# Optimization experiments

Measured on AMD Instinct MI355X. Metric: run time of the kernel, lower is better.

## Reference

```python
import jax, jax.numpy as jnp
import numpy as np

W_DIM = 512
CHANNELS = 1024
SIZE = 64            # H = W = 64
SAMPLING_RATE = 64.0
BANDWIDTH = 2.0


def setup_inputs() -> dict:
    key = jax.random.key(0)
    k_w, k_f, k_p, k_wt, k_aw = jax.random.split(key, 5)
    B = 16
    w = jax.random.normal(k_w, (B, W_DIM), dtype=jnp.float32)
    # freqs init as in SynthesisInput.__init__
    freqs = jax.random.normal(k_f, (CHANNELS, 2), dtype=jnp.float32)
    radii = jnp.sqrt(jnp.sum(freqs ** 2, axis=1, keepdims=True))
    freqs = freqs / (radii * jnp.exp(radii ** 2) ** 0.25) * BANDWIDTH
    phases = jax.random.uniform(k_p, (CHANNELS,), dtype=jnp.float32) - 0.5
    weight = jax.random.normal(k_wt, (CHANNELS, CHANNELS), dtype=jnp.float32)
    # affine FC layer (weight_init=0 in original; use small random for a useful test)
    affine_w = jax.random.normal(k_aw, (4, W_DIM), dtype=jnp.float32) * 0.1
    affine_b = jnp.array([1.0, 0.0, 0.0, 0.0], dtype=jnp.float32)
    return {"w": w, "freqs": freqs, "phases": phases, "weight": weight,
            "affine_w": affine_w, "affine_b": affine_b}


def _forward(w, freqs, phases, weight, affine_w, affine_b):
    B = w.shape[0]
    C = freqs.shape[0]
    H = Wd = SIZE
    # affine: FullyConnectedLayer gain = 1/sqrt(in_features)
    t = w @ affine_w.T / jnp.sqrt(jnp.float32(W_DIM)) + affine_b  # [B,4]
    t = t / jnp.linalg.norm(t[:, :2], axis=1, keepdims=True)
    c, s = t[:, 0], t[:, 1]
    # rotation block of m_r (identity base transform, so transform_ = m_r @ m_t)
    R = jnp.stack([jnp.stack([c, -s], -1), jnp.stack([s, c], -1)], -2)  # [B,2,2]
    # translation column: transform_[:, :2, 2] = R @ (-t[:,2:4])
    trans_col = -jnp.einsum('bij,bj->bi', R, t[:, 2:4])                 # [B,2]
    phases_b = phases[None, :] + jnp.einsum('cd,bd->bc', freqs, trans_col)  # [B,C]
    freqs_b = jnp.einsum('cd,bde->bce', freqs, R)                           # [B,C,2]
    amps = jnp.clip(
        1.0 - (jnp.linalg.norm(freqs_b, axis=2) - BANDWIDTH)
        / (SAMPLING_RATE / 2 - BANDWIDTH), 0.0, 1.0)                        # [B,C]
    # affine_grid (align_corners=False): normalized coords (2i+1)/N - 1, scaled
    sx = 0.5 * Wd / SAMPLING_RATE
    sy = 0.5 * H / SAMPLING_RATE
    u = ((jnp.arange(Wd, dtype=jnp.float32) + 0.5) / Wd * 2.0 - 1.0) * sx  # x (width)
    v = ((jnp.arange(H, dtype=jnp.float32) + 0.5) / H * 2.0 - 1.0) * sy    # y (height)
    grid = jnp.stack(jnp.meshgrid(u, v, indexing='xy'), axis=-1)           # [H,W,2]
    x = jnp.einsum('hwd,bcd->bhwc', grid, freqs_b) + phases_b[:, None, None, :]
    x = jnp.sin(x * (2.0 * jnp.pi)) * amps[:, None, None, :]
    x = jnp.einsum('bhwc,kc->bhwk', x, weight / jnp.sqrt(jnp.float32(C)))
    return jnp.transpose(x, (0, 3, 1, 2))  # [B,C,H,W]


def reference(w, freqs, phases, weight, affine_w, affine_b):
    return _forward(w, freqs, phases, weight, affine_w, affine_b)
```

## Files before the change

### kernel.cpp

```cpp
#include <hip/hip_runtime.h>

typedef __attribute__((ext_vector_type(4))) float f32x4;
typedef __attribute__((ext_vector_type(8))) short s16x8;
typedef __attribute__((ext_vector_type(8))) unsigned short u16x8;

#define W_DIM   512
#define CHANNELS 1024
#define SPATIAL 4096
#define NB      16

__device__ inline unsigned short f2bf(float x){
  unsigned int u = __float_as_uint(x);
  u += 0x7fffu + ((u >> 16) & 1u);
  return (unsigned short)(u >> 16);
}

__device__ inline float sin2pi(float x){
  return __builtin_amdgcn_sinf(__builtin_amdgcn_fractf(x));
}
__device__ inline float cos2pi(float x){
  return __builtin_amdgcn_cosf(__builtin_amdgcn_fractf(x));
}

__device__ inline void async_load16(const unsigned short* g, unsigned short* l){
  __builtin_amdgcn_global_load_lds(
      (const __attribute__((address_space(1))) void*)g,
      (__attribute__((address_space(3))) void*)l, 16, 0, 0);
}

__global__ void sy_setup(const float* __restrict__ w, const float* __restrict__ freqs,
                         const float* __restrict__ phases, const float* __restrict__ affine_w,
                         const float* __restrict__ affine_b, float4* __restrict__ params){
  int b = blockIdx.x;
  int t = threadIdx.x;
  float p0=0.f, p1=0.f, p2=0.f, p3=0.f;
  #pragma unroll
  for (int it = 0; it < 2; ++it){
    int i = t + it*256;
    float wv = w[b*W_DIM + i];
    p0 += wv * affine_w[0*W_DIM + i];
    p1 += wv * affine_w[1*W_DIM + i];
    p2 += wv * affine_w[2*W_DIM + i];
    p3 += wv * affine_w[3*W_DIM + i];
  }
  #pragma unroll
  for (int off = 32; off >= 1; off >>= 1){
    p0 += __shfl_down(p0, off);
    p1 += __shfl_down(p1, off);
    p2 += __shfl_down(p2, off);
    p3 += __shfl_down(p3, off);
  }
  __shared__ float red[4][4];
  __shared__ float sc[4];
  int wave = t >> 6, lane = t & 63;
  if (lane == 0){ red[wave][0]=p0; red[wave][1]=p1; red[wave][2]=p2; red[wave][3]=p3; }
  __syncthreads();
  if (t == 0){
    const float inv_sq = 0.04419417382415922f;
    float tv[4];
    #pragma unroll
    for (int j=0;j<4;++j){
      float s = red[0][j]+red[1][j]+red[2][j]+red[3][j];
      tv[j] = s * inv_sq + affine_b[j];
    }
    float n  = sqrtf(tv[0]*tv[0] + tv[1]*tv[1]);
    float iv = 1.0f / n;
    float c = tv[0]*iv, s = tv[1]*iv;
    float t2 = tv[2]*iv, t3 = tv[3]*iv;
    float tcx = -(c*t2 - s*t3);
    float tcy = -(s*t2 + c*t3);
    sc[0]=c; sc[1]=s; sc[2]=tcx; sc[3]=tcy;
  }
  __syncthreads();
  float c = sc[0], s = sc[1], tcx = sc[2], tcy = sc[3];
  #pragma unroll
  for (int j = 0; j < 4; ++j){
    int ci = t + j*256;
    float f0x = freqs[ci*2], f0y = freqs[ci*2+1];
    float fx =  f0x*c + f0y*s;
    float fy = -f0x*s + f0y*c;
    float ph = phases[ci] + f0x*tcx + f0y*tcy;
    float r  = sqrtf(fx*fx + fy*fy);
    float amp = 1.0f - (r - 2.0f) * (1.0f/30.0f);
    amp = fminf(fmaxf(amp, 0.0f), 1.0f);
    float4 P; P.x=fx; P.y=fy; P.z=ph; P.w=amp;
    params[b*CHANNELS + ci] = P;
  }
}

__global__ void sy_cvtw(const float* __restrict__ wt, unsigned short* __restrict__ Wbf){
  int i = (blockIdx.x*256 + threadIdx.x)*4;
  float4 v = *(const float4*)(wt + i);
  ushort4 o;
  o.x = f2bf(v.x*0.03125f); o.y = f2bf(v.y*0.03125f);
  o.z = f2bf(v.z*0.03125f); o.w = f2bf(v.w*0.03125f);
  *(ushort4*)(Wbf + i) = o;
}

__global__ void sy_genS(const float4* __restrict__ params, unsigned short* __restrict__ Sbf,
                        int b0){
  int blk = blockIdx.x;
  int bb  = blk >> 7;
  int b   = b0 + bb;
  int m0  = (blk & 127) * 32;
  int t   = threadIdx.x;
  int c0  = (t & 127) * 8;
  int mh  = t >> 7;
  int h   = m0 >> 6;
  int w0  = (m0 + mh*16) & 63;
  float v  = (h  + 0.5f) * (1.0f/64.0f) - 0.5f;
  float u0 = (w0 + 0.5f) * (1.0f/64.0f) - 0.5f;

  float sU[8], cU[8], sV[8], cV[8], sD[8], cD[8];
  #pragma unroll
  for (int j = 0; j < 8; ++j){
    float4 P = params[b*CHANNELS + c0 + j];
    float V = v*P.y + P.z;
    sV[j] = sin2pi(V) * P.w;
    cV[j] = cos2pi(V) * P.w;
    float U = u0*P.x;
    sU[j] = sin2pi(U);
    cU[j] = cos2pi(U);
    float D = P.x * (1.0f/64.0f);
    sD[j] = sin2pi(D);
    cD[j] = cos2pi(D);
  }

  unsigned short* dst = Sbf + ((size_t)bb * SPATIAL + m0 + mh*16) * CHANNELS + c0;
  for (int im = 0; im < 16; ++im){
    u16x8 o;
    #pragma unroll
    for (int j = 0; j < 8; ++j){
      float val = sU[j]*cV[j] + cU[j]*sV[j];
      o[j] = f2bf(val);
      float ns = sU[j]*cD[j] + cU[j]*sD[j];
      float nc = cU[j]*cD[j] - sU[j]*sD[j];
      sU[j] = ns; cU[j] = nc;
    }
    *(u16x8*)(dst + (size_t)im * CHANNELS) = o;
  }
}

__global__ __launch_bounds__(512, 4) void sy_gemm(const unsigned short* __restrict__ Wbf,
                                                  const unsigned short* __restrict__ Sbf,
                                                  float* __restrict__ out, int b0){
  __shared__ __align__(16) unsigned short lds[3][12288];
  const int tid  = threadIdx.x;
  const int lane = tid & 63, wave = tid >> 6;
  const int wm = wave >> 1, wn = wave & 1;

  const int nwg = gridDim.x;
  const int cpx = nwg >> 3;
  const int bid = blockIdx.x;
  const int sbid = (bid & 7)*cpx + (bid >> 3);
  const int mt  = sbid & 3;
  const int ntl = sbid >> 2;
  const size_t NcolL = (size_t)ntl * 128;
  const int bbl = (int)(NcolL >> 12);
  const int nin = (int)(NcolL & 4095);
  const unsigned short* Abase = Wbf + (size_t)mt * 256 * CHANNELS;
  const unsigned short* Bbase = Sbf + NcolL * CHANNELS;

  int voffA[2], loffA[2];
  #pragma unroll
  for (int j = 0; j < 2; ++j){
    int p   = j*512 + tid;
    int row = p >> 2;
    int kc  = (p & 3) ^ ((row >> 1) & 3);
    voffA[j] = row*CHANNELS + kc*8;
    loffA[j] = p*8;
  }
  int voffB, loffB;
  {
    int p   = tid;
    int row = p >> 2;
    int kc  = (p & 3) ^ ((row >> 1) & 3);
    voffB   = row*CHANNELS + kc*8;
    loffB   = 8192 + p*8;
  }

  const int l15 = lane & 15, kg = lane >> 4;
  const int xs  = (kg ^ ((l15 >> 1) & 3)) * 8;
  const int aoff =        (wm*64 + l15)*32 + xs;
  const int boff = 8192 + (wn*64 + l15)*32 + xs;

  f32x4 acc[4][4];
  #pragma unroll
  for (int i=0;i<4;++i)
    #pragma unroll
    for (int j=0;j<4;++j){
      f32x4 z = {0.f,0.f,0.f,0.f};
      acc[i][j] = z;
    }

  auto STAGE = [&](int kt, int s){
    const int ko = kt * 32;
    unsigned short* l = &lds[s][0];
    async_load16(Abase + voffA[0] + ko, l + loffA[0]);
    async_load16(Abase + voffA[1] + ko, l + loffA[1]);
    async_load16(Bbase + voffB   + ko, l + loffB);
  };
  auto COMPUTE = [&](int s){
    const unsigned short* l = &lds[s][0];
    s16x8 af[4], bv[4];
    #pragma unroll
    for (int i=0;i<4;++i) af[i] = *(const s16x8*)&l[aoff + i*512];
    #pragma unroll
    for (int j=0;j<4;++j) bv[j] = *(const s16x8*)&l[boff + j*512];
    __builtin_amdgcn_s_setprio(1);
    #pragma unroll
    for (int i=0;i<4;++i)
      #pragma unroll
      for (int j=0;j<4;++j)
        acc[i][j] = __builtin_amdgcn_mfma_f32_16x16x32_bf16(af[i], bv[j], acc[i][j], 0, 0, 0);
    __builtin_amdgcn_s_setprio(0);
  };

  STAGE(0, 0); STAGE(1, 1);
  asm volatile("s_waitcnt vmcnt(3)" ::: "memory");
  __builtin_amdgcn_s_barrier();

  int sc = 0, ss = 2;
  for (int t = 0; t < 30; ++t){
    STAGE(t + 2, ss);
    COMPUTE(sc);
    asm volatile("s_waitcnt vmcnt(3)" ::: "memory");
    __builtin_amdgcn_s_barrier();
    sc = (sc == 2) ? 0 : sc + 1;
    ss = (ss == 2) ? 0 : ss + 1;
  }
  COMPUTE(sc);
  asm volatile("s_waitcnt vmcnt(0)" ::: "memory");
  __builtin_amdgcn_s_barrier();
  COMPUTE(1);

  float* outb = out + (size_t)(b0 + bbl) * CHANNELS * SPATIAL;
  const int colb = nin + wn*64 + l15;
  const int row0 = mt*256 + wm*64 + (kg << 2);
  #pragma unroll
  for (int mf = 0; mf < 4; ++mf)
    #pragma unroll
    for (int nf = 0; nf < 4; ++nf)
      #pragma unroll
      for (int r = 0; r < 4; ++r)
        outb[(size_t)(row0 + mf*16 + r) * SPATIAL + colb + nf*16] = acc[mf][nf][r];
}

__global__ void sy_fallback(const float* __restrict__ weight, const float4* __restrict__ params,
                            float* __restrict__ out){
  extern __shared__ float S[];
  int b  = blockIdx.x >> 7;
  int m0 = (blockIdx.x & 127) * 32;
  int t  = threadIdx.x;
  {
    int c0 = t*4;
    float4 P0 = params[b*CHANNELS+c0+0], P1 = params[b*CHANNELS+c0+1];
    float4 P2 = params[b*CHANNELS+c0+2], P3 = params[b*CHANNELS+c0+3];
    int h = m0 >> 6;
    float v = (h + 0.5f)*(1.0f/64.0f) - 0.5f;
    float a0 = v*P0.y+P0.z, a1 = v*P1.y+P1.z, a2 = v*P2.y+P2.z, a3 = v*P3.y+P3.z;
    for (int im = 0; im < 32; ++im){
      int wv = (m0+im) & 63;
      float u = (wv+0.5f)*(1.0f/64.0f) - 0.5f;
      float* row = S + im*CHANNELS + c0;
      row[0] = sin2pi(u*P0.x+a0)*P0.w;
      row[1] = sin2pi(u*P1.x+a1)*P1.w;
      row[2] = sin2pi(u*P2.x+a2)*P2.w;
      row[3] = sin2pi(u*P3.x+a3)*P3.w;
    }
  }
  __syncthreads();
  for (int oi = t; oi < 32*1024; oi += 256){
    int k = oi >> 5, im = oi & 31;
    const float4* wr = (const float4*)(weight + (size_t)k*CHANNELS);
    const float4* sr = (const float4*)(S + im*CHANNELS);
    float sum = 0.f;
    for (int c4 = 0; c4 < CHANNELS/4; ++c4){
      float4 a = wr[c4], s4 = sr[c4];
      sum += a.x*s4.x + a.y*s4.y + a.z*s4.z + a.w*s4.w;
    }
    out[((size_t)b*CHANNELS + k)*SPATIAL + m0 + im] = sum * 0.03125f;
  }
}

extern "C" void kernel_launch(void* const* d_in, const int* in_sizes, int n_in,
                              void* d_out, int out_size, void* d_ws, size_t ws_size,
                              hipStream_t stream){
  const float* w        = (const float*)d_in[0];
  const float* freqs    = (const float*)d_in[1];
  const float* phases   = (const float*)d_in[2];
  const float* weight   = (const float*)d_in[3];
  const float* affine_w = (const float*)d_in[4];
  const float* affine_b = (const float*)d_in[5];
  float* out = (float*)d_out;

  char* ws = (char*)d_ws;
  float4* params = (float4*)ws;
  const size_t off_w = 262144;
  const size_t off_s = off_w + 2097152;
  unsigned short* Wbf = (unsigned short*)(ws + off_w);
  unsigned short* Sbf = (unsigned short*)(ws + off_s);
  const size_t per_batch = (size_t)SPATIAL * CHANNELS * 2;

  sy_setup<<<NB, 256, 0, stream>>>(w, freqs, phases, affine_w, affine_b, params);

  int G = 0;
  if (ws_size >= off_s + per_batch){
    size_t avail = (ws_size - off_s) / per_batch;
    G = avail >= (size_t)NB ? NB : (int)avail;
  }
  if (G == 0){
    sy_fallback<<<NB*128, 256, 32*1024*4, stream>>>(weight, params, out);
    return;
  }
  sy_cvtw<<<1024, 256, 0, stream>>>(weight, Wbf);
  for (int b0 = 0; b0 < NB; b0 += G){
    int g = (NB - b0) < G ? (NB - b0) : G;
    sy_genS<<<g*128, 256, 0, stream>>>(params, Sbf, b0);
    sy_gemm<<<g*128, 512, 0, stream>>>(Wbf, Sbf, out, b0);
  }
}
```

Before: 439.3 us.

## Fuse sinusoid feature generation into GEMM producer, drop global S buffer

Removes the separate sy_genS kernel and its 128 MB bf16 intermediate. Each GEMM workgroup now computes its B-operand tile of sin features directly into shared memory, one K-slice per iteration, using the rotation recurrence. The GEMM tile also grows from 256x128 to 256x256 with a 4-deep A buffer and a 2-deep B buffer, and occupancy drops to 2 workgroups. This saves the global write and reread of the feature matrix, at the cost of per-iteration transcendental work, scattered 2-byte LDS stores and higher register pressure from 32 accumulators per wave.

Result: no change. 440.3 us (+0.2%).

```diff
diff --git a/kernel.cpp b/kernel.cpp
--- a/kernel.cpp
+++ b/kernel.cpp
@@ -2,7 +2,6 @@
 
 typedef __attribute__((ext_vector_type(4))) float f32x4;
 typedef __attribute__((ext_vector_type(8))) short s16x8;
-typedef __attribute__((ext_vector_type(8))) unsigned short u16x8;
 
 #define W_DIM   512
 #define CHANNELS 1024
@@ -97,57 +96,14 @@
   *(ushort4*)(Wbf + i) = o;
 }
 
-__global__ void sy_genS(const float4* __restrict__ params, unsigned short* __restrict__ Sbf,
-                        int b0){
-  int blk = blockIdx.x;
-  int bb  = blk >> 7;
-  int b   = b0 + bb;
-  int m0  = (blk & 127) * 32;
-  int t   = threadIdx.x;
-  int c0  = (t & 127) * 8;
-  int mh  = t >> 7;
-  int h   = m0 >> 6;
-  int w0  = (m0 + mh*16) & 63;
-  float v  = (h  + 0.5f) * (1.0f/64.0f) - 0.5f;
-  float u0 = (w0 + 0.5f) * (1.0f/64.0f) - 0.5f;
-
-  float sU[8], cU[8], sV[8], cV[8], sD[8], cD[8];
-  #pragma unroll
-  for (int j = 0; j < 8; ++j){
-    float4 P = params[b*CHANNELS + c0 + j];
-    float V = v*P.y + P.z;
-    sV[j] = sin2pi(V) * P.w;
-    cV[j] = cos2pi(V) * P.w;
-    float U = u0*P.x;
-    sU[j] = sin2pi(U);
-    cU[j] = cos2pi(U);
-    float D = P.x * (1.0f/64.0f);
-    sD[j] = sin2pi(D);
-    cD[j] = cos2pi(D);
-  }
-
-  unsigned short* dst = Sbf + ((size_t)bb * SPATIAL + m0 + mh*16) * CHANNELS + c0;
-  for (int im = 0; im < 16; ++im){
-    u16x8 o;
-    #pragma unroll
-    for (int j = 0; j < 8; ++j){
-      float val = sU[j]*cV[j] + cU[j]*sV[j];
-      o[j] = f2bf(val);
-      float ns = sU[j]*cD[j] + cU[j]*sD[j];
-      float nc = cU[j]*cD[j] - sU[j]*sD[j];
-      sU[j] = ns; cU[j] = nc;
-    }
-    *(u16x8*)(dst + (size_t)im * CHANNELS) = o;
-  }
-}
-
-__global__ __launch_bounds__(512, 4) void sy_gemm(const unsigned short* __restrict__ Wbf,
-                                                  const unsigned short* __restrict__ Sbf,
-                                                  float* __restrict__ out, int b0){
-  __shared__ __align__(16) unsigned short lds[3][12288];
+__global__ __launch_bounds__(512, 2) void sy_gemm(const unsigned short* __restrict__ Wbf,
+                                                  const float4* __restrict__ params,
+                                                  float* __restrict__ out){
+  __shared__ __align__(16) unsigned short ldsA[4][8192];
+  __shared__ __align__(16) unsigned short ldsB[2][8192];
   const int tid  = threadIdx.x;
   const int lane = tid & 63, wave = tid >> 6;
-  const int wm = wave >> 1, wn = wave & 1;
+  const int wm = wave >> 2, wn = wave & 3;
 
   const int nwg = gridDim.x;
   const int cpx = nwg >> 3;
@@ -155,90 +111,116 @@
   const int sbid = (bid & 7)*cpx + (bid >> 3);
   const int mt  = sbid & 3;
   const int ntl = sbid >> 2;
-  const size_t NcolL = (size_t)ntl * 128;
-  const int bbl = (int)(NcolL >> 12);
+  const size_t NcolL = (size_t)ntl * 256;
+  const int b   = (int)(NcolL >> 12);
   const int nin = (int)(NcolL & 4095);
   const unsigned short* Abase = Wbf + (size_t)mt * 256 * CHANNELS;
-  const unsigned short* Bbase = Sbf + NcolL * CHANNELS;
-
-  int voffA[2], loffA[2];
+
+  int voff[2], loff[2];
   #pragma unroll
   for (int j = 0; j < 2; ++j){
-    int p   = j*512 + tid;
+    int p   = (j*8 + wave)*64 + lane;
     int row = p >> 2;
     int kc  = (p & 3) ^ ((row >> 1) & 3);
-    voffA[j] = row*CHANNELS + kc*8;
-    loffA[j] = p*8;
-  }
-  int voffB, loffB;
-  {
-    int p   = tid;
-    int row = p >> 2;
-    int kc  = (p & 3) ^ ((row >> 1) & 3);
-    voffB   = row*CHANNELS + kc*8;
-    loffB   = 8192 + p*8;
-  }
+    voff[j] = row*CHANNELS + kc*8;
+    loff[j] = p*8;
+  }
+
+  const int chl  = tid & 31;
+  const int hw   = tid >> 5;
+  const int hloc = hw >> 2, wseg = hw & 3;
+  const int colbase = hloc*64 + wseg*16;
+  const int hglob = (nin >> 6) + hloc;
+  const float v  = (hglob + 0.5f)*(1.0f/64.0f) - 0.5f;
+  const float u0 = (wseg*16 + 0.5f)*(1.0f/64.0f) - 0.5f;
+  const int ch7 = chl & 7, cgc = chl >> 3;
+  const float4* Pb = params + (size_t)b*CHANNELS + chl;
 
   const int l15 = lane & 15, kg = lane >> 4;
   const int xs  = (kg ^ ((l15 >> 1) & 3)) * 8;
-  const int aoff =        (wm*64 + l15)*32 + xs;
-  const int boff = 8192 + (wn*64 + l15)*32 + xs;
-
-  f32x4 acc[4][4];
-  #pragma unroll
-  for (int i=0;i<4;++i)
+  const int aoff = (wm*128 + l15)*32 + xs;
+  const int boff = (wn*64  + l15)*32 + xs;
+
+  f32x4 acc[8][4];
+  #pragma unroll
+  for (int i=0;i<8;++i)
     #pragma unroll
     for (int j=0;j<4;++j){
       f32x4 z = {0.f,0.f,0.f,0.f};
       acc[i][j] = z;
     }
 
-  auto STAGE = [&](int kt, int s){
-    const int ko = kt * 32;
-    unsigned short* l = &lds[s][0];
-    async_load16(Abase + voffA[0] + ko, l + loffA[0]);
-    async_load16(Abase + voffA[1] + ko, l + loffA[1]);
-    async_load16(Bbase + voffB   + ko, l + loffB);
+  auto STAGE = [&](int kt){
+    const int ko = kt*32;
+    unsigned short* la = &ldsA[kt & 3][0];
+    async_load16(Abase + voff[0] + ko, la + loff[0]);
+    async_load16(Abase + voff[1] + ko, la + loff[1]);
   };
-  auto COMPUTE = [&](int s){
-    const unsigned short* l = &lds[s][0];
-    s16x8 af[4], bv[4];
-    #pragma unroll
-    for (int i=0;i<4;++i) af[i] = *(const s16x8*)&l[aoff + i*512];
-    #pragma unroll
-    for (int j=0;j<4;++j) bv[j] = *(const s16x8*)&l[boff + j*512];
+  auto SGEN = [&](int kt){
+    float4 P = Pb[kt*32];
+    float V  = v*P.y + P.z;
+    float sV = sin2pi(V)*P.w, cV = cos2pi(V)*P.w;
+    float U  = u0*P.x;
+    float sU = sin2pi(U), cU = cos2pi(U);
+    float D  = P.x * (1.0f/64.0f);
+    float sD = sin2pi(D), cD = cos2pi(D);
+    unsigned short* bl = &ldsB[kt & 1][0];
+    #pragma unroll
+    for (int i = 0; i < 16; ++i){
+      int col = colbase + i;
+      int cl  = cgc ^ ((col >> 1) & 3);
+      bl[col*32 + cl*8 + ch7] = f2bf(sU*cV + cU*sV);
+      float ns = sU*cD + cU*sD;
+      float nc = cU*cD - sU*sD;
+      sU = ns; cU = nc;
+    }
+  };
+  auto COMPUTE = [&](int sA, int sB){
+    s16x8 af[8], bv[4];
+    #pragma unroll
+    for (int mf=0; mf<8; ++mf) af[mf] = *(const s16x8*)&ldsA[sA][aoff + mf*512];
+    #pragma unroll
+    for (int nf=0; nf<4; ++nf) bv[nf] = *(const s16x8*)&ldsB[sB][boff + nf*512];
     __builtin_amdgcn_s_setprio(1);
     #pragma unroll
-    for (int i=0;i<4;++i)
+    for (int mf=0; mf<8; ++mf)
       #pragma unroll
-      for (int j=0;j<4;++j)
-        acc[i][j] = __builtin_amdgcn_mfma_f32_16x16x32_bf16(af[i], bv[j], acc[i][j], 0, 0, 0);
+      for (int nf=0; nf<4; ++nf)
+        acc[mf][nf] = __builtin_amdgcn_mfma_f32_16x16x32_bf16(af[mf], bv[nf], acc[mf][nf], 0, 0, 0);
     __builtin_amdgcn_s_setprio(0);
   };
 
-  STAGE(0, 0); STAGE(1, 1);
-  asm volatile("s_waitcnt vmcnt(3)" ::: "memory");
+  SGEN(0);
+  STAGE(0); STAGE(1); STAGE(2);
+  asm volatile("s_waitcnt lgkmcnt(0)" ::: "memory");
+  asm volatile("s_waitcnt vmcnt(4)"   ::: "memory");
   __builtin_amdgcn_s_barrier();
 
-  int sc = 0, ss = 2;
-  for (int t = 0; t < 30; ++t){
-    STAGE(t + 2, ss);
-    COMPUTE(sc);
-    asm volatile("s_waitcnt vmcnt(3)" ::: "memory");
+  for (int t = 0; t < 29; ++t){
+    SGEN(t + 1);
+    STAGE(t + 3);
+    COMPUTE(t & 3, t & 1);
+    asm volatile("s_waitcnt lgkmcnt(0)" ::: "memory");
+    asm volatile("s_waitcnt vmcnt(4)"   ::: "memory");
     __builtin_amdgcn_s_barrier();
-    sc = (sc == 2) ? 0 : sc + 1;
-    ss = (ss == 2) ? 0 : ss + 1;
-  }
-  COMPUTE(sc);
-  asm volatile("s_waitcnt vmcnt(0)" ::: "memory");
+  }
+  SGEN(30);
+  COMPUTE(29 & 3, 29 & 1);
+  asm volatile("s_waitcnt lgkmcnt(0)" ::: "memory");
+  asm volatile("s_waitcnt vmcnt(2)"   ::: "memory");
   __builtin_amdgcn_s_barrier();
-  COMPUTE(1);
-
-  float* outb = out + (size_t)(b0 + bbl) * CHANNELS * SPATIAL;
+  SGEN(31);
+  COMPUTE(30 & 3, 30 & 1);
+  asm volatile("s_waitcnt lgkmcnt(0)" ::: "memory");
+  asm volatile("s_waitcnt vmcnt(0)"   ::: "memory");
+  __builtin_amdgcn_s_barrier();
+  COMPUTE(31 & 3, 31 & 1);
+
+  float* outb = out + (size_t)b * CHANNELS * SPATIAL;
   const int colb = nin + wn*64 + l15;
-  const int row0 = mt*256 + wm*64 + (kg << 2);
-  #pragma unroll
-  for (int mf = 0; mf < 4; ++mf)
+  const int row0 = mt*256 + wm*128 + (kg << 2);
+  #pragma unroll
+  for (int mf = 0; mf < 8; ++mf)
     #pragma unroll
     for (int nf = 0; nf < 4; ++nf)
       #pragma unroll
@@ -297,26 +279,14 @@
   char* ws = (char*)d_ws;
   float4* params = (float4*)ws;
   const size_t off_w = 262144;
-  const size_t off_s = off_w + 2097152;
   unsigned short* Wbf = (unsigned short*)(ws + off_w);
-  unsigned short* Sbf = (unsigned short*)(ws + off_s);
-  const size_t per_batch = (size_t)SPATIAL * CHANNELS * 2;
 
   sy_setup<<<NB, 256, 0, stream>>>(w, freqs, phases, affine_w, affine_b, params);
 
-  int G = 0;
-  if (ws_size >= off_s + per_batch){
-    size_t avail = (ws_size - off_s) / per_batch;
-    G = avail >= (size_t)NB ? NB : (int)avail;
-  }
-  if (G == 0){
+  if (ws_size >= off_w + 2097152){
+    sy_cvtw<<<1024, 256, 0, stream>>>(weight, Wbf);
+    sy_gemm<<<NB*64, 512, 0, stream>>>(Wbf, params, out);
+  } else {
     sy_fallback<<<NB*128, 256, 32*1024*4, stream>>>(weight, params, out);
-    return;
-  }
-  sy_cvtw<<<1024, 256, 0, stream>>>(weight, Wbf);
-  for (int b0 = 0; b0 < NB; b0 += G){
-    int g = (NB - b0) < G ? (NB - b0) : G;
-    sy_genS<<<g*128, 256, 0, stream>>>(params, Sbf, b0);
-    sy_gemm<<<g*128, 512, 0, stream>>>(Wbf, Sbf, out, b0);
-  }
-}
+  }
+}
```

## Enlarge GEMM tile to 256x256 with 4-stage LDS pipeline

Applied to the files above, without the earlier changes.

Doubles the GEMM block's N tile from 128 to 256 columns, giving each wave a 128x64 sub-tile with 32 accumulators, and halves the grid. The LDS ring goes from 3 to 4 stages with a 3-deep prefetch, so loads run further ahead of compute. Each tile load is reused across more MFMAs, but register pressure rises (launch bounds cut to 2 blocks per CU), occupancy drops, and there are fewer workgroups to spread across CUs.

Measured after the change: 428.5 us. 2.5% less time.

```diff
diff --git a/kernel.cpp b/kernel.cpp
--- a/kernel.cpp
+++ b/kernel.cpp
@@ -141,13 +141,13 @@
   }
 }
 
-__global__ __launch_bounds__(512, 4) void sy_gemm(const unsigned short* __restrict__ Wbf,
+__global__ __launch_bounds__(512, 2) void sy_gemm(const unsigned short* __restrict__ Wbf,
                                                   const unsigned short* __restrict__ Sbf,
                                                   float* __restrict__ out, int b0){
-  __shared__ __align__(16) unsigned short lds[3][12288];
+  __shared__ __align__(16) unsigned short lds[4][2][8192];
   const int tid  = threadIdx.x;
   const int lane = tid & 63, wave = tid >> 6;
-  const int wm = wave >> 1, wn = wave & 1;
+  const int wm = wave >> 2, wn = wave & 3;
 
   const int nwg = gridDim.x;
   const int cpx = nwg >> 3;
@@ -155,90 +155,84 @@
   const int sbid = (bid & 7)*cpx + (bid >> 3);
   const int mt  = sbid & 3;
   const int ntl = sbid >> 2;
-  const size_t NcolL = (size_t)ntl * 128;
+  const size_t NcolL = (size_t)ntl * 256;
   const int bbl = (int)(NcolL >> 12);
   const int nin = (int)(NcolL & 4095);
   const unsigned short* Abase = Wbf + (size_t)mt * 256 * CHANNELS;
   const unsigned short* Bbase = Sbf + NcolL * CHANNELS;
 
-  int voffA[2], loffA[2];
+  int voff[2], loff[2];
   #pragma unroll
   for (int j = 0; j < 2; ++j){
-    int p   = j*512 + tid;
+    int p   = (j*8 + wave)*64 + lane;
     int row = p >> 2;
-    int kc  = (p & 3) ^ ((row >> 1) & 3);
-    voffA[j] = row*CHANNELS + kc*8;
-    loffA[j] = p*8;
-  }
-  int voffB, loffB;
-  {
-    int p   = tid;
-    int row = p >> 2;
-    int kc  = (p & 3) ^ ((row >> 1) & 3);
-    voffB   = row*CHANNELS + kc*8;
-    loffB   = 8192 + p*8;
+    int kcg = (p & 3) ^ ((row >> 1) & 3);
+    voff[j] = row*CHANNELS + kcg*8;
+    loff[j] = p*8;
   }
 
   const int l15 = lane & 15, kg = lane >> 4;
   const int xs  = (kg ^ ((l15 >> 1) & 3)) * 8;
-  const int aoff =        (wm*64 + l15)*32 + xs;
-  const int boff = 8192 + (wn*64 + l15)*32 + xs;
-
-  f32x4 acc[4][4];
-  #pragma unroll
-  for (int i=0;i<4;++i)
+  const int aoff = (wm*128 + l15)*32 + xs;
+  const int boff = (wn*64  + l15)*32 + xs;
+
+  f32x4 acc[8][4];
+  #pragma unroll
+  for (int i=0;i<8;++i)
     #pragma unroll
     for (int j=0;j<4;++j){
       f32x4 z = {0.f,0.f,0.f,0.f};
       acc[i][j] = z;
     }
 
-  auto STAGE = [&](int kt, int s){
-    const int ko = kt * 32;
-    unsigned short* l = &lds[s][0];
-    async_load16(Abase + voffA[0] + ko, l + loffA[0]);
-    async_load16(Abase + voffA[1] + ko, l + loffA[1]);
-    async_load16(Bbase + voffB   + ko, l + loffB);
+  auto STAGE = [&](int kt){
+    const int ko = kt*32;
+    unsigned short* la = (unsigned short*)&lds[kt & 3][0][0];
+    unsigned short* lb = (unsigned short*)&lds[kt & 3][1][0];
+    #pragma unroll
+    for (int j = 0; j < 2; ++j){
+      async_load16(Abase + voff[j] + ko, la + loff[j]);
+      async_load16(Bbase + voff[j] + ko, lb + loff[j]);
+    }
   };
   auto COMPUTE = [&](int s){
-    const unsigned short* l = &lds[s][0];
-    s16x8 af[4], bv[4];
-    #pragma unroll
-    for (int i=0;i<4;++i) af[i] = *(const s16x8*)&l[aoff + i*512];
-    #pragma unroll
-    for (int j=0;j<4;++j) bv[j] = *(const s16x8*)&l[boff + j*512];
+    s16x8 af[8], bv[4];
+    #pragma unroll
+    for (int mf = 0; mf < 8; ++mf) af[mf] = *(const s16x8*)&lds[s][0][aoff + mf*512];
+    #pragma unroll
+    for (int nf = 0; nf < 4; ++nf) bv[nf] = *(const s16x8*)&lds[s][1][boff + nf*512];
     __builtin_amdgcn_s_setprio(1);
     #pragma unroll
-    for (int i=0;i<4;++i)
+    for (int mf = 0; mf < 8; ++mf)
       #pragma unroll
-      for (int j=0;j<4;++j)
-        acc[i][j] = __builtin_amdgcn_mfma_f32_16x16x32_bf16(af[i], bv[j], acc[i][j], 0, 0, 0);
+      for (int nf = 0; nf < 4; ++nf)
+        acc[mf][nf] = __builtin_amdgcn_mfma_f32_16x16x32_bf16(af[mf], bv[nf], acc[mf][nf], 0, 0, 0);
     __builtin_amdgcn_s_setprio(0);
   };
 
-  STAGE(0, 0); STAGE(1, 1);
-  asm volatile("s_waitcnt vmcnt(3)" ::: "memory");
+  STAGE(0); STAGE(1); STAGE(2);
+  asm volatile("s_waitcnt vmcnt(8)" ::: "memory");
   __builtin_amdgcn_s_barrier();
 
-  int sc = 0, ss = 2;
-  for (int t = 0; t < 30; ++t){
-    STAGE(t + 2, ss);
-    COMPUTE(sc);
-    asm volatile("s_waitcnt vmcnt(3)" ::: "memory");
+  for (int t = 0; t < 29; ++t){
+    STAGE(t + 3);
+    COMPUTE(t & 3);
+    asm volatile("s_waitcnt vmcnt(8)" ::: "memory");
     __builtin_amdgcn_s_barrier();
-    sc = (sc == 2) ? 0 : sc + 1;
-    ss = (ss == 2) ? 0 : ss + 1;
-  }
-  COMPUTE(sc);
+  }
+  COMPUTE(29 & 3);
+  asm volatile("s_waitcnt vmcnt(4)" ::: "memory");
+  __builtin_amdgcn_s_barrier();
+  COMPUTE(30 & 3);
   asm volatile("s_waitcnt vmcnt(0)" ::: "memory");
   __builtin_amdgcn_s_barrier();
-  COMPUTE(1);
+  COMPUTE(31 & 3);
 
   float* outb = out + (size_t)(b0 + bbl) * CHANNELS * SPATIAL;
   const int colb = nin + wn*64 + l15;
-  const int row0 = mt*256 + wm*64 + (kg << 2);
-  #pragma unroll
-  for (int mf = 0; mf < 4; ++mf)
+  const int row0 = mt*256 + wm*128 + (kg << 2);
+  #pragma unroll
+  for (int mf = 0; mf < 8; ++mf)
     #pragma unroll
     for (int nf = 0; nf < 4; ++nf)
       #pragma unroll
@@ -317,6 +311,6 @@
   for (int b0 = 0; b0 < NB; b0 += G){
     int g = (NB - b0) < G ? (NB - b0) : G;
     sy_genS<<<g*128, 256, 0, stream>>>(params, Sbf, b0);
-    sy_gemm<<<g*128, 512, 0, stream>>>(Wbf, Sbf, out, b0);
-  }
-}
+    sy_gemm<<<g*64, 512, 0, stream>>>(Wbf, Sbf, out, b0);
+  }
+}
```
